# Kernel optimization log

Hardware: AMD Instinct MI355X
Metric: run time of the kernel (lower is better)

## Reference

```python
import jax, jax.numpy as jnp
import numpy as np

B, T, F, H, D, NC = 4096, 16, 64, 512, 15, 2  # batch, seq, feat(+time), hidden, mem window, classes
FX = F - 1  # real feature dim (channel 0 is the time delta)


def setup_inputs() -> dict:
    key = jax.random.key(0)
    ks = jax.random.split(key, 24)
    u = lambda k, shape, s=0.05: jax.random.uniform(k, shape, jnp.float32, -s, s)
    return {
        "inputs": jax.random.normal(ks[0], (B, T, F), jnp.float32),
        "init_proj": u(ks[1], (F, H)),            # self._init, keras random_uniform
        "hc_init": jnp.zeros((1, H), jnp.float32),  # h/c init (zeros initializer)
        # TH_cell: fused LSTM gates [i,f,o,c]
        "Wx": u(ks[2], (FX, 4 * H)),
        "Uh": u(ks[3], (H, 4 * H)),
        "Wt": u(ks[4], (1, 3 * H)),               # time delta -> i,f,o gates
        "b": jnp.zeros((4 * H,), jnp.float32),
        # time-aware gate
        "WxT": u(ks[5], (FX, H)),
        "WtT": u(ks[6], (1, H)),
        "bT": jnp.zeros((H,), jnp.float32),
        # historical attention over str_mem
        "Wa": u(ks[7], (H, H)),
        "Wb": u(ks[8], (H, H)),
        "va": u(ks[9], (H,)),
        "ba": jnp.zeros((H,), jnp.float32),
        # interaction / output combine
        "We": u(ks[10], (H, H)),
        "Wg": u(ks[11], (H, H)),
        "bh": jnp.zeros((H,), jnp.float32),
        # classifier head (Dropout is identity at inference)
        "W1": u(ks[12], (H, 256)),
        "b1": jnp.zeros((256,), jnp.float32),
        "W2": u(ks[13], (256, 32)),
        "b2": jnp.zeros((32,), jnp.float32),
        "W3": u(ks[14], (32, NC)),
        "b3": jnp.zeros((NC,), jnp.float32),
    }


def reference(inputs, init_proj, hc_init, Wx, Uh, Wt, b, WxT, WtT, bT,
              Wa, Wb, va, ba, We, Wg, bh, W1, b1, W2, b2, W3, b3):
    Bn = inputs.shape[0]
    # str_mem init: ones_like(inputs) @ _init, drop last step -> [B, T-1=D, H]
    str_mem = jnp.matmul(jnp.ones_like(inputs), init_proj)[:, :-1]
    h = jnp.broadcast_to(hc_init, (Bn, H))
    c = jnp.broadcast_to(hc_init, (Bn, H))
    x_seq = jnp.transpose(inputs[..., 1:], (1, 0, 2))   # [T, B, FX]
    t_seq = jnp.transpose(inputs[..., :1], (1, 0, 2))   # [T, B, 1]

    def step(carry, xt):
        h, c, mem = carry
        x, t = xt
        z = x @ Wx + h @ Uh + b                      # [B, 4H]
        zi, zf, zo, zc = jnp.split(z, 4, axis=-1)
        ti, tf_, to = jnp.split(t @ Wt, 3, axis=-1)
        i = jax.nn.sigmoid(zi + ti)
        f = jax.nn.sigmoid(zf + tf_)
        o = jax.nn.sigmoid(zo + to)
        chat = jnp.tanh(zc)
        Tg = jax.nn.sigmoid(x @ WxT + jax.nn.sigmoid(t @ WtT) + bT)  # time-aware gate
        c_new = f * c + i * chat + Tg * chat
        h_cur = o * jnp.tanh(c_new)
        # historical attention over sliding memory [B, D, H]
        e = jnp.einsum('bdh,h->bd',
                       jnp.tanh(jnp.einsum('bdh,hk->bdk', mem, Wa)
                                + (h_cur @ Wb + ba)[:, None, :]), va)
        alpha = jax.nn.softmax(e, axis=1)
        ctx = jnp.einsum('bd,bdh->bh', alpha, mem)
        h_new = jnp.tanh(ctx @ We + h_cur @ Wg + bh)
        mem_new = jnp.concatenate([mem[:, 1:], h_new[:, None]], axis=1)
        return (h_new, c_new, mem_new), None

    (h, c, str_mem), _ = jax.lax.scan(step, (h, c, str_mem), (x_seq, t_seq))
    hd = jax.nn.relu(h @ W1 + b1)
    hd = jax.nn.relu(hd @ W2 + b2)
    return jax.nn.softmax(hd @ W3 + b3, axis=-1)
```

## Files before the change

kernel.cpp:

```cpp
#include <hip/hip_runtime.h>
#include <hip/hip_bf16.h>

typedef __bf16 bf16;
typedef __attribute__((ext_vector_type(8))) __bf16 bf16x8;
typedef __attribute__((ext_vector_type(4))) float floatx4;

#define HDIM 512
#define BATCH 4096
#define TSTEPS 16
#define KA 576
#define NR 3584

typedef const __attribute__((address_space(1))) void gvoid;
typedef __attribute__((address_space(3))) void svoid;

__device__ __forceinline__ float ftanh2(float x) {
  return fmaf(-2.f, __builtin_amdgcn_rcpf(exp2f(x * 2.8853900817779268f) + 1.f), 1.f);
}
__device__ __forceinline__ float fsigm2(float x) {
  return __builtin_amdgcn_rcpf(1.f + exp2f(-x * 1.4426950408889634f));
}

__device__ __forceinline__ float waveAllSum(float v) {
#pragma unroll
  for (int off = 32; off > 0; off >>= 1) v += __shfl_xor(v, off, 64);
  return v;
}

__global__ __launch_bounds__(256, 4)
void gemm1_fused(const bf16* __restrict__ A1, const bf16* __restrict__ A2,
                 const bf16* __restrict__ BT,
                 const float* __restrict__ tdT, const float* __restrict__ bvec,
                 const float* __restrict__ WtT, const float* __restrict__ bT,
                 float* __restrict__ cbuf, bf16* __restrict__ hcur,
                 bf16* __restrict__ waSlot, bf16* __restrict__ weSlot) {
  constexpr int BM = 128, BN = 112, BK = 64;
  constexpr int TM = 2, TN = 7;
  __shared__ __align__(16) bf16 As[BM * BK];
  __shared__ __align__(16) bf16 Bs[BN * BK];

  const int tid = threadIdx.x;
  const int lane = tid & 63;
  const int wv = tid >> 6;
  const int quad = lane >> 4;
  const int lr = lane & 15;
  const int bid = blockIdx.x;
  const int xcd = bid & 7;
  const int p = bid >> 3;
  const int n_idx = (xcd << 2) | (p >> 5);
  const int m_idx = p & 31;
  const int m0 = m_idx * BM;
  const int n0 = n_idx * BN;
  const int g8 = lane >> 3;
  const int cl = (lane & 7) ^ g8;

  floatx4 acc[TM][TN];
#pragma unroll
  for (int i = 0; i < TM; ++i)
#pragma unroll
    for (int j = 0; j < TN; ++j) {
      acc[i][j][0] = 0.f; acc[i][j][1] = 0.f; acc[i][j][2] = 0.f; acc[i][j][3] = 0.f;
    }

  {
#pragma unroll
    for (int s = 0; s < 4; ++s) {
      const int g = wv * 4 + s;
      const int r = g * 8 + g8;
      const bf16* src = A1 + (size_t)(m0 + r) * 64 + cl * 8;
      __builtin_amdgcn_global_load_lds((gvoid*)src, (svoid*)&As[g * 512], 16, 0, 0);
    }
#pragma unroll
    for (int s = 0; s < 4; ++s) {
      const int g = wv * 4 + s;
      if (g < 10) {
        const int r = g * 8 + g8;
        const bf16* src = BT + (size_t)(n0 + r) * KA + cl * 8;
        __builtin_amdgcn_global_load_lds((gvoid*)src, (svoid*)&Bs[g * 512], 16, 0, 0);
      }
    }
    __syncthreads();
#pragma unroll
    for (int s = 0; s < 2; ++s) {
      const int lc = s * 4 + quad;
      bf16x8 afr[TM];
      bf16x8 bfr[5];
#pragma unroll
      for (int i = 0; i < TM; ++i) {
        const int r = wv * 32 + i * 16 + lr;
        afr[i] = *reinterpret_cast<const bf16x8*>(&As[r * 64 + ((lc ^ (r & 7)) << 3)]);
      }
#pragma unroll
      for (int j = 0; j < 5; ++j) {
        const int r = j * 16 + lr;
        bfr[j] = *reinterpret_cast<const bf16x8*>(&Bs[r * 64 + ((lc ^ (r & 7)) << 3)]);
      }
#pragma unroll
      for (int i = 0; i < TM; ++i)
#pragma unroll
        for (int j = 0; j < 5; ++j)
          acc[i][j] = __builtin_amdgcn_mfma_f32_16x16x32_bf16(afr[i], bfr[j], acc[i][j], 0, 0, 0);
    }
  }

  constexpr int JMAP[6] = {0, 1, 2, 3, 5, 6};
  for (int kt = 1; kt < KA / BK; ++kt) {
    const int kb = kt * BK;
    __syncthreads();
#pragma unroll
    for (int s = 0; s < 4; ++s) {
      const int g = wv * 4 + s;
      const int r = g * 8 + g8;
      const bf16* src = A2 + (size_t)(m0 + r) * 512 + (kb - 64) + cl * 8;
      __builtin_amdgcn_global_load_lds((gvoid*)src, (svoid*)&As[g * 512], 16, 0, 0);
    }
#pragma unroll
    for (int s = 0; s < 4; ++s) {
      const int g = wv * 4 + s;
      if (g < 14 && g != 8 && g != 9) {
        const int r = g * 8 + g8;
        const bf16* src = BT + (size_t)(n0 + r) * KA + kb + cl * 8;
        __builtin_amdgcn_global_load_lds((gvoid*)src, (svoid*)&Bs[g * 512], 16, 0, 0);
      }
    }
    __syncthreads();
#pragma unroll
    for (int s = 0; s < 2; ++s) {
      const int lc = s * 4 + quad;
      bf16x8 afr[TM];
      bf16x8 bfr[6];
#pragma unroll
      for (int i = 0; i < TM; ++i) {
        const int r = wv * 32 + i * 16 + lr;
        afr[i] = *reinterpret_cast<const bf16x8*>(&As[r * 64 + ((lc ^ (r & 7)) << 3)]);
      }
#pragma unroll
      for (int jj = 0; jj < 6; ++jj) {
        const int r = JMAP[jj] * 16 + lr;
        bfr[jj] = *reinterpret_cast<const bf16x8*>(&Bs[r * 64 + ((lc ^ (r & 7)) << 3)]);
      }
#pragma unroll
      for (int i = 0; i < TM; ++i)
#pragma unroll
        for (int jj = 0; jj < 6; ++jj)
          acc[i][JMAP[jj]] =
              __builtin_amdgcn_mfma_f32_16x16x32_bf16(afr[i], bfr[jj], acc[i][JMAP[jj]], 0, 0, 0);
    }
  }

  const int hcol = n_idx * 16 + lr;
  const float bvi = bvec[hcol], bvf = bvec[512 + hcol];
  const float bvo = bvec[1024 + hcol], bvc = bvec[1536 + hcol];
  const float wtt = WtT[hcol], bt_ = bT[hcol];
#pragma unroll
  for (int i = 0; i < TM; ++i) {
#pragma unroll
    for (int r = 0; r < 4; ++r) {
      const int m = m0 + wv * 32 + i * 16 + quad * 4 + r;
      const float td = tdT[m];
      const size_t o = (size_t)m * 512 + hcol;
      const float c_old = cbuf[o];
      const float i_ = fsigm2(acc[i][0][r] + bvi);
      const float f_ = fsigm2(acc[i][1][r] + bvf);
      const float o_ = fsigm2(acc[i][2][r] + bvo);
      const float ch = ftanh2(acc[i][3][r] + bvc);
      const float tg = fsigm2(acc[i][4][r] + fsigm2(td * wtt) + bt_);
      const float cn = f_ * c_old + (i_ + tg) * ch;
      cbuf[o] = cn;
      hcur[o] = (bf16)(o_ * ftanh2(cn));
      waSlot[o] = (bf16)acc[i][5][r];
      weSlot[o] = (bf16)acc[i][6][r];
    }
  }
}

__global__ __launch_bounds__(256, 4)
void gemm2_kernel(const bf16* __restrict__ hcur, const bf16* __restrict__ wbwgT,
                  const float* __restrict__ baPad, bf16* __restrict__ hWbG) {
  __shared__ __align__(16) bf16 As[128 * 64];
  __shared__ __align__(16) bf16 Bs[64 * 64];

  const int tid = threadIdx.x;
  const int lane = tid & 63;
  const int wv = tid >> 6;
  const int quad = lane >> 4;
  const int lr = lane & 15;
  const int bid = blockIdx.x;
  const int m0 = (bid >> 4) * 128;
  const int n0 = (bid & 15) * 64;
  const int g8 = lane >> 3;
  const int cl = (lane & 7) ^ g8;

  floatx4 acc[2][4];
#pragma unroll
  for (int i = 0; i < 2; ++i)
#pragma unroll
    for (int j = 0; j < 4; ++j) {
      acc[i][j][0] = 0.f; acc[i][j][1] = 0.f; acc[i][j][2] = 0.f; acc[i][j][3] = 0.f;
    }

  for (int kt = 0; kt < 8; ++kt) {
    const int kb = kt * 64;
    __syncthreads();
#pragma unroll
    for (int s = 0; s < 4; ++s) {
      const int g = wv * 4 + s;
      const int r = g * 8 + g8;
      const bf16* src = hcur + (size_t)(m0 + r) * 512 + kb + cl * 8;
      __builtin_amdgcn_global_load_lds((gvoid*)src, (svoid*)&As[g * 512], 16, 0, 0);
    }
#pragma unroll
    for (int s = 0; s < 2; ++s) {
      const int g = wv * 2 + s;
      const int r = g * 8 + g8;
      const bf16* src = wbwgT + (size_t)(n0 + r) * 512 + kb + cl * 8;
      __builtin_amdgcn_global_load_lds((gvoid*)src, (svoid*)&Bs[g * 512], 16, 0, 0);
    }
    __syncthreads();
#pragma unroll
    for (int s = 0; s < 2; ++s) {
      const int lc = s * 4 + quad;
      bf16x8 afr[2];
      bf16x8 bfr[4];
#pragma unroll
      for (int i = 0; i < 2; ++i) {
        const int r = wv * 32 + i * 16 + lr;
        afr[i] = *reinterpret_cast<const bf16x8*>(&As[r * 64 + ((lc ^ (r & 7)) << 3)]);
      }
#pragma unroll
      for (int j = 0; j < 4; ++j) {
        const int r = j * 16 + lr;
        bfr[j] = *reinterpret_cast<const bf16x8*>(&Bs[r * 64 + ((lc ^ (r & 7)) << 3)]);
      }
#pragma unroll
      for (int i = 0; i < 2; ++i)
#pragma unroll
        for (int j = 0; j < 4; ++j)
          acc[i][j] = __builtin_amdgcn_mfma_f32_16x16x32_bf16(afr[i], bfr[j], acc[i][j], 0, 0, 0);
    }
  }

#pragma unroll
  for (int i = 0; i < 2; ++i) {
#pragma unroll
    for (int j = 0; j < 4; ++j) {
      const int n = n0 + j * 16 + lr;
      const float bb = baPad[n];
#pragma unroll
      for (int r = 0; r < 4; ++r) {
        const int m = m0 + wv * 32 + i * 16 + quad * 4 + r;
        hWbG[(size_t)m * 1024 + n] = (bf16)(acc[i][j][r] + bb);
      }
    }
  }
}

template <int BM, int BN>
__global__ __launch_bounds__(256)
void gemm_glds_kernel(const bf16* __restrict__ A1, int ld1, int K1,
                      const bf16* __restrict__ A2, int ld2,
                      const bf16* __restrict__ BT, int K, int mode,
                      float* __restrict__ outF, int ldF, const float* __restrict__ colBias,
                      bf16* __restrict__ outBa, int ldBa, const float* __restrict__ cBias2) {
  constexpr int BK = 32;
  constexpr int WM = BM / 2;
  constexpr int WN = BN / 2;
  constexpr int TM = WM / 16;
  constexpr int TN = WN / 16;
  constexpr int AIW = BM / 64;
  constexpr int BIW = BN / 64;
  __shared__ __align__(16) bf16 As[BM * BK];
  __shared__ __align__(16) bf16 Bs[BN * BK];

  const int tid = threadIdx.x;
  const int lane = tid & 63;
  const int wv = tid >> 6;
  const int wy = wv >> 1;
  const int wx = wv & 1;
  const int quad = lane >> 4;
  const int lr = lane & 15;
  const int m0 = blockIdx.y * BM;
  const int n0 = blockIdx.x * BN;
  const int sw = quad ^ ((lr >> 1) & 3);
  const int srow = lane >> 2;
  const int cl = (lane & 3) ^ ((lane >> 3) & 3);

  floatx4 acc[TM][TN];
#pragma unroll
  for (int i = 0; i < TM; ++i)
#pragma unroll
    for (int j = 0; j < TN; ++j) {
      acc[i][j][0] = 0.f; acc[i][j][1] = 0.f; acc[i][j][2] = 0.f; acc[i][j][3] = 0.f;
    }

  const int kTiles = K / BK;
  for (int kt = 0; kt < kTiles; ++kt) {
    const int kb = kt * BK;
    __syncthreads();
#pragma unroll
    for (int s = 0; s < AIW; ++s) {
      const int rbase = (wv * AIW + s) * 16;
      const int r = rbase + srow;
      const int col = kb + cl * 8;
      const bf16* src = (col < K1) ? (A1 + (size_t)(m0 + r) * ld1 + col)
                                   : (A2 + (size_t)(m0 + r) * ld2 + (col - K1));
      __builtin_amdgcn_global_load_lds((gvoid*)src, (svoid*)&As[rbase * BK], 16, 0, 0);
    }
#pragma unroll
    for (int s = 0; s < BIW; ++s) {
      const int rbase = (wv * BIW + s) * 16;
      const int r = rbase + srow;
      const bf16* src = BT + (size_t)(n0 + r) * K + kb + cl * 8;
      __builtin_amdgcn_global_load_lds((gvoid*)src, (svoid*)&Bs[rbase * BK], 16, 0, 0);
    }
    __syncthreads();
    bf16x8 afr[TM];
    bf16x8 bfr[TN];
#pragma unroll
    for (int i = 0; i < TM; ++i)
      afr[i] = *reinterpret_cast<const bf16x8*>(&As[(wy * WM + i * 16 + lr) * BK + sw * 8]);
#pragma unroll
    for (int j = 0; j < TN; ++j)
      bfr[j] = *reinterpret_cast<const bf16x8*>(&Bs[(wx * WN + j * 16 + lr) * BK + sw * 8]);
#pragma unroll
    for (int i = 0; i < TM; ++i)
#pragma unroll
      for (int j = 0; j < TN; ++j)
        acc[i][j] = __builtin_amdgcn_mfma_f32_16x16x32_bf16(afr[i], bfr[j], acc[i][j], 0, 0, 0);
  }

#pragma unroll
  for (int i = 0; i < TM; ++i) {
#pragma unroll
    for (int j = 0; j < TN; ++j) {
#pragma unroll
      for (int r = 0; r < 4; ++r) {
        int m = m0 + wy * WM + i * 16 + quad * 4 + r;
        int n = n0 + wx * WN + j * 16 + lr;
        float v = acc[i][j][r];
        if (mode == 0) {
          if (colBias != nullptr) v += colBias[n];
          outF[(size_t)m * ldF + n] = v;
        } else {
          v += cBias2[n];
          v = v > 0.f ? v : 0.f;
          outBa[(size_t)m * ldBa + n] = (bf16)v;
        }
      }
    }
  }
}

__global__ void pack_wcombT_kernel(const float* __restrict__ Wx, const float* __restrict__ Uh,
                                   const float* __restrict__ Wt, const float* __restrict__ WxT,
                                   const float* __restrict__ Wa, const float* __restrict__ We,
                                   bf16* __restrict__ out) {
  int idx = blockIdx.x * 256 + threadIdx.x;
  if (idx >= NR * KA) return;
  int n = idx / KA;
  int k = idx - n * KA;
  int blk = n / 112;
  int rem = n - blk * 112;
  int role = rem >> 4;
  int h = blk * 16 + (rem & 15);
  float v = 0.f;
  if (k < 63) {
    if (role < 4) v = Wx[k * 2048 + role * 512 + h];
    else if (role == 4) v = WxT[k * 512 + h];
  } else if (k == 63) {
    if (role < 3) v = Wt[role * 512 + h];
  } else {
    int kh = k - 64;
    if (role < 4) v = Uh[kh * 2048 + role * 512 + h];
    else if (role == 5) v = Wa[kh * 512 + h];
    else if (role == 6) v = We[kh * 512 + h];
  }
  out[idx] = (bf16)v;
}

__global__ void pack_t_kernel(const float* __restrict__ in, bf16* __restrict__ out, int N, int K) {
  int idx = blockIdx.x * 256 + threadIdx.x;
  if (idx >= N * K) return;
  int n = idx / K;
  int j = idx - n * K;
  out[idx] = (bf16)in[(size_t)j * N + n];
}

__global__ __launch_bounds__(512)
void setup_misc_kernel(const float* __restrict__ init_proj, const float* __restrict__ Wa,
                       const float* __restrict__ We, const float* __restrict__ ba,
                       float* __restrict__ sWa, float* __restrict__ sWe,
                       float* __restrict__ baPad) {
  __shared__ float s_sh[HDIM];
  int h = threadIdx.x;
  float acc = 0.f;
  for (int f = 0; f < 64; ++f) acc += init_proj[f * HDIM + h];
  s_sh[h] = acc;
  baPad[h] = ba[h];
  baPad[HDIM + h] = 0.f;
  __syncthreads();
  float a2 = 0.f, a3 = 0.f;
  for (int i = 0; i < HDIM; ++i) {
    a2 += s_sh[i] * Wa[i * HDIM + h];
    a3 += s_sh[i] * We[i * HDIM + h];
  }
  sWa[h] = a2;
  sWe[h] = a3;
}

__global__ void zero_state_kernel(float* __restrict__ c, bf16* __restrict__ h) {
  int idx = blockIdx.x * 256 + threadIdx.x;
  if (idx >= BATCH * HDIM) return;
  c[idx] = 0.f;
  h[idx] = (bf16)0.f;
}

__global__ void build_x_kernel(const float* __restrict__ inputs, bf16* __restrict__ xbuf,
                               float* __restrict__ tdT) {
  int idx = blockIdx.x * 256 + threadIdx.x;
  if (idx >= TSTEPS * BATCH * 64) return;
  int c = idx & 63;
  int bt = idx >> 6;
  int t = bt >> 12;
  int b = bt & 4095;
  float v;
  if (c < 63) {
    v = inputs[(size_t)b * 1024 + t * 64 + 1 + c];
  } else {
    v = inputs[(size_t)b * 1024 + t * 64];
    tdT[t * BATCH + b] = v;
  }
  xbuf[idx] = (bf16)v;
}

template <int K>
__global__ __launch_bounds__(256, 4)
void attention_kernel(const bf16* __restrict__ hWbG,
                      const float* __restrict__ sWa, const float* __restrict__ sWe,
                      const float* __restrict__ va, const float* __restrict__ bh,
                      const bf16* __restrict__ histWa, const bf16* __restrict__ histWe,
                      bf16* __restrict__ hbuf) {
  constexpr float C = 2.8853900817779268f;
  constexpr float L2E = 1.4426950408889634f;
  constexpr int CH = 4;
  constexpr int NC = (K + CH - 1) / CH;
  const int b = blockIdx.x * 4 + (threadIdx.x >> 6);
  const int lane = threadIdx.x & 63;
  const bf16* wbp = hWbG + (size_t)b * 1024 + lane * 8;
  bf16x8 wbv = *reinterpret_cast<const bf16x8*>(wbp);
  bf16x8 wgv = *reinterpret_cast<const bf16x8*>(wbp + 512);

  const bf16* pa = histWa + (size_t)b * HDIM + lane * 8;
  const bf16* pe = histWe + (size_t)b * HDIM + lane * 8;
  constexpr size_t RSTR = (size_t)BATCH * HDIM;

  bf16x8 buf[2][CH];
  if (NC > 0) {
#pragma unroll
    for (int r = 0; r < CH; ++r)
      if (r < K) buf[0][r] = *reinterpret_cast<const bf16x8*>(pa + (size_t)r * RSTR);
    asm volatile("" ::: "memory");
  }

  float wb2[8], vv[8];
  float svv = 0.f;
#pragma unroll
  for (int i = 0; i < 8; ++i) {
    wb2[i] = (float)wbv[i] * C;
    vv[i] = va[lane * 8 + i];
    svv += vv[i];
  }

  float e_init = 0.f;
  if (K < 15) {
    float p = 0.f;
#pragma unroll
    for (int i = 0; i < 8; ++i) {
      float r = __builtin_amdgcn_rcpf(exp2f(fmaf(sWa[lane * 8 + i], C, wb2[i])) + 1.f);
      p = fmaf(vv[i], r, p);
    }
    e_init = waveAllSum(fmaf(-2.f, p, svv));
  }

  float q[K > 0 ? K : 1];
#pragma unroll
  for (int c = 0; c < NC; ++c) {
    if (c + 1 < NC) {
#pragma unroll
      for (int r = 0; r < CH; ++r) {
        const int j = (c + 1) * CH + r;
        if (j < K)
          buf[(c + 1) & 1][r] = *reinterpret_cast<const bf16x8*>(pa + (size_t)j * RSTR);
      }
      asm volatile("" ::: "memory");
    }
#pragma unroll
    for (int r = 0; r < CH; ++r) {
      const int j = c * CH + r;
      if (j < K) {
        float p = 0.f;
#pragma unroll
        for (int i = 0; i < 8; ++i) {
          float t = __builtin_amdgcn_rcpf(
              exp2f(fmaf((float)buf[c & 1][r][i], C, wb2[i])) + 1.f);
          p = fmaf(vv[i], t, p);
        }
        q[j] = fmaf(-2.f, p, svv);
      }
    }
  }

  bf16x8 ebuf[2][CH];
  if (NC > 0) {
#pragma unroll
    for (int r = 0; r < CH; ++r)
      if (r < K) ebuf[0][r] = *reinterpret_cast<const bf16x8*>(pe + (size_t)r * RSTR);
    asm volatile("" ::: "memory");
  }

#pragma unroll
  for (int off = 32; off > 0; off >>= 1) {
#pragma unroll
    for (int j = 0; j < K; ++j) q[j] += __shfl_xor(q[j], off, 64);
  }

  float mx = (K < 15) ? e_init : -1e30f;
#pragma unroll
  for (int j = 0; j < K; ++j) mx = fmaxf(mx, q[j]);
  float winit = (K < 15) ? (float)(15 - K) * exp2f((e_init - mx) * L2E) : 0.f;
  float denom = winit;
  float w[K > 0 ? K : 1];
#pragma unroll
  for (int j = 0; j < K; ++j) {
    w[j] = exp2f((q[j] - mx) * L2E);
    denom += w[j];
  }
  const float inv = __builtin_amdgcn_rcpf(denom);

  float cx[8];
  const float ai = winit * inv;
#pragma unroll
  for (int i = 0; i < 8; ++i) cx[i] = ai * sWe[lane * 8 + i];
#pragma unroll
  for (int c = 0; c < NC; ++c) {
    if (c + 1 < NC) {
#pragma unroll
      for (int r = 0; r < CH; ++r) {
        const int j = (c + 1) * CH + r;
        if (j < K)
          ebuf[(c + 1) & 1][r] = *reinterpret_cast<const bf16x8*>(pe + (size_t)j * RSTR);
      }
      asm volatile("" ::: "memory");
    }
#pragma unroll
    for (int r = 0; r < CH; ++r) {
      const int j = c * CH + r;
      if (j < K) {
        const float aj = w[j] * inv;
#pragma unroll
        for (int i = 0; i < 8; ++i) cx[i] = fmaf(aj, (float)ebuf[c & 1][r][i], cx[i]);
      }
    }
  }

  bf16x8 hnew;
#pragma unroll
  for (int i = 0; i < 8; ++i) {
    float s = cx[i] + (float)wgv[i] + bh[lane * 8 + i];
    float r = __builtin_amdgcn_rcpf(exp2f(s * C) + 1.f);
    hnew[i] = (bf16)fmaf(-2.f, r, 1.f);
  }
  *reinterpret_cast<bf16x8*>(hbuf + (size_t)b * HDIM + lane * 8) = hnew;
}

__global__ __launch_bounds__(256)
void head_kernel(const bf16* __restrict__ hd1, const float* __restrict__ W2,
                 const float* __restrict__ b2, const float* __restrict__ W3,
                 const float* __restrict__ b3, float* __restrict__ out) {
  __shared__ float W2s[256 * 32];
  __shared__ float b2s[32];
  __shared__ float W3s[64];
  __shared__ float b3s[2];
  for (int i = threadIdx.x; i < 256 * 32; i += 256) W2s[i] = W2[i];
  if (threadIdx.x < 32) b2s[threadIdx.x] = b2[threadIdx.x];
  if (threadIdx.x < 64) W3s[threadIdx.x] = W3[threadIdx.x];
  if (threadIdx.x < 2) b3s[threadIdx.x] = b3[threadIdx.x];
  __syncthreads();
  int row = blockIdx.x * 256 + threadIdx.x;
  float acc[32];
#pragma unroll
  for (int j = 0; j < 32; ++j) acc[j] = b2s[j];
  const bf16* hp = hd1 + (size_t)row * 256;
  for (int i = 0; i < 256; ++i) {
    float hv = (float)hp[i];
#pragma unroll
    for (int j = 0; j < 32; ++j) acc[j] += hv * W2s[i * 32 + j];
  }
  float l0 = b3s[0], l1 = b3s[1];
#pragma unroll
  for (int j = 0; j < 32; ++j) {
    float r = fmaxf(acc[j], 0.f);
    l0 += r * W3s[j * 2];
    l1 += r * W3s[j * 2 + 1];
  }
  float m = fmaxf(l0, l1);
  float e0 = __expf(l0 - m), e1 = __expf(l1 - m);
  float inv = 1.f / (e0 + e1);
  out[(size_t)row * 2] = e0 * inv;
  out[(size_t)row * 2 + 1] = e1 * inv;
}

extern "C" void kernel_launch(void* const* d_in, const int* in_sizes, int n_in,
                              void* d_out, int out_size, void* d_ws, size_t ws_size,
                              hipStream_t stream) {
  const float* inputs    = (const float*)d_in[0];
  const float* init_proj = (const float*)d_in[1];
  const float* Wx  = (const float*)d_in[3];
  const float* Uh  = (const float*)d_in[4];
  const float* Wt  = (const float*)d_in[5];
  const float* bv  = (const float*)d_in[6];
  const float* WxT = (const float*)d_in[7];
  const float* WtT = (const float*)d_in[8];
  const float* bT  = (const float*)d_in[9];
  const float* Wa  = (const float*)d_in[10];
  const float* Wb  = (const float*)d_in[11];
  const float* va  = (const float*)d_in[12];
  const float* ba  = (const float*)d_in[13];
  const float* We  = (const float*)d_in[14];
  const float* Wg  = (const float*)d_in[15];
  const float* bh  = (const float*)d_in[16];
  const float* W1  = (const float*)d_in[17];
  const float* b1  = (const float*)d_in[18];
  const float* W2  = (const float*)d_in[19];
  const float* b2  = (const float*)d_in[20];
  const float* W3  = (const float*)d_in[21];
  const float* b3  = (const float*)d_in[22];
  float* out = (float*)d_out;

  char* wp = (char*)d_ws;
  auto carve = [&](size_t bytes) -> void* {
    void* p = (void*)wp;
    wp += (bytes + 255) & ~(size_t)255;
    return p;
  };
  bf16* wcombT = (bf16*)carve((size_t)NR * KA * 2);
  bf16* wbwgT  = (bf16*)carve((size_t)1024 * 512 * 2);
  bf16* w1T    = (bf16*)carve((size_t)256 * 512 * 2);
  float* sWa   = (float*)carve(512 * 4);
  float* sWe   = (float*)carve(512 * 4);
  float* baPad = (float*)carve(1024 * 4);
  bf16* xbuf   = (bf16*)carve((size_t)TSTEPS * BATCH * 64 * 2);
  float* tdT   = (float*)carve((size_t)TSTEPS * BATCH * 4);
  float* cbuf  = (float*)carve((size_t)BATCH * HDIM * 4);
  bf16* hbuf   = (bf16*)carve((size_t)BATCH * HDIM * 2);
  bf16* hcur   = (bf16*)carve((size_t)BATCH * HDIM * 2);
  bf16* hWbG   = (bf16*)carve((size_t)BATCH * 1024 * 2);
  bf16* histWa = (bf16*)carve((size_t)16 * BATCH * HDIM * 2);
  bf16* histWe = (bf16*)carve((size_t)16 * BATCH * HDIM * 2);
  bf16* hd1    = (bf16*)carve((size_t)BATCH * 256 * 2);

  build_x_kernel<<<(TSTEPS * BATCH * 64) / 256, 256, 0, stream>>>(inputs, xbuf, tdT);
  pack_wcombT_kernel<<<(NR * KA + 255) / 256, 256, 0, stream>>>(Wx, Uh, Wt, WxT, Wa, We, wcombT);
  pack_t_kernel<<<(512 * 512) / 256, 256, 0, stream>>>(Wb, wbwgT, 512, 512);
  pack_t_kernel<<<(512 * 512) / 256, 256, 0, stream>>>(Wg, wbwgT + (size_t)512 * 512, 512, 512);
  pack_t_kernel<<<(256 * 512) / 256, 256, 0, stream>>>(W1, w1T, 256, 512);
  setup_misc_kernel<<<1, 512, 0, stream>>>(init_proj, Wa, We, ba, sWa, sWe, baPad);
  zero_state_kernel<<<(BATCH * HDIM) / 256, 256, 0, stream>>>(cbuf, hbuf);

#define ATTN_LAUNCH(KK)                                                              \
  case KK:                                                                           \
    attention_kernel<KK><<<BATCH / 4, 256, 0, stream>>>(hWbG, sWa, sWe, va, bh,      \
                                                        histWa, histWe, hbuf);       \
    break;

  for (int t = 0; t < TSTEPS; ++t) {
    bf16* waSlot = histWa + (size_t)((t + 15) & 15) * BATCH * HDIM;
    bf16* weSlot = histWe + (size_t)((t + 15) & 15) * BATCH * HDIM;
    gemm1_fused<<<1024, 256, 0, stream>>>(
        xbuf + (size_t)t * BATCH * 64, hbuf, wcombT, tdT + (size_t)t * BATCH, bv, WtT, bT,
        cbuf, hcur, waSlot, weSlot);
    gemm2_kernel<<<512, 256, 0, stream>>>(hcur, wbwgT, baPad, hWbG);
    switch (t) {
      ATTN_LAUNCH(0) ATTN_LAUNCH(1) ATTN_LAUNCH(2) ATTN_LAUNCH(3)
      ATTN_LAUNCH(4) ATTN_LAUNCH(5) ATTN_LAUNCH(6) ATTN_LAUNCH(7)
      ATTN_LAUNCH(8) ATTN_LAUNCH(9) ATTN_LAUNCH(10) ATTN_LAUNCH(11)
      ATTN_LAUNCH(12) ATTN_LAUNCH(13) ATTN_LAUNCH(14) ATTN_LAUNCH(15)
    }
  }
#undef ATTN_LAUNCH

  gemm_glds_kernel<64, 128><<<dim3(256 / 128, BATCH / 64), 256, 0, stream>>>(
      hbuf, 512, 512, hbuf, 512, w1T, 512, 3, nullptr, 0, nullptr, hd1, 256, b1);
  head_kernel<<<BATCH / 256, 256, 0, stream>>>(hd1, W2, b2, W3, b3, out);
}
```

Before: 987.0 us.

## Split attention memory slots across two waves per batch row

The attention kernel now assigns two waves to each batch row, with each wave handling alternate memory slots (even or odd j). Partial scores are exchanged through shared memory for the softmax, and the second wave's partial context vector is combined through shared memory before the final tanh. The grid doubles and the launch-bounds occupancy hint rises from 4 to 5. This halves per-wave serial load and exp work and register pressure, aiming to hide memory latency better. The cost is two block-wide barriers, extra LDS traffic, and recomputing the exp weights in both waves.

```diff
diff --git a/kernel.cpp b/kernel.cpp
--- a/kernel.cpp
+++ b/kernel.cpp
@@ -434,7 +434,7 @@
 }
 
 template <int K>
-__global__ __launch_bounds__(256, 4)
+__global__ __launch_bounds__(256, 5)
 void attention_kernel(const bf16* __restrict__ hWbG,
                       const float* __restrict__ sWa, const float* __restrict__ sWe,
                       const float* __restrict__ va, const float* __restrict__ bh,
@@ -443,9 +443,18 @@
   constexpr float C = 2.8853900817779268f;
   constexpr float L2E = 1.4426950408889634f;
   constexpr int CH = 4;
-  constexpr int NC = (K + CH - 1) / CH;
-  const int b = blockIdx.x * 4 + (threadIdx.x >> 6);
-  const int lane = threadIdx.x & 63;
+  constexpr int MAXJ = (K + 1) / 2;
+  constexpr int NC = (MAXJ + CH - 1) / CH;
+  __shared__ float qsh[2][16];
+  __shared__ float cxsh[2][8 * 64];
+
+  const int tid = threadIdx.x;
+  const int lane = tid & 63;
+  const int wv = tid >> 6;
+  const int br = wv >> 1;
+  const int half = wv & 1;
+  const int b = blockIdx.x * 2 + br;
+
   const bf16* wbp = hWbG + (size_t)b * 1024 + lane * 8;
   bf16x8 wbv = *reinterpret_cast<const bf16x8*>(wbp);
   bf16x8 wgv = *reinterpret_cast<const bf16x8*>(wbp + 512);
@@ -454,11 +463,15 @@
   const bf16* pe = histWe + (size_t)b * HDIM + lane * 8;
   constexpr size_t RSTR = (size_t)BATCH * HDIM;
 
-  bf16x8 buf[2][CH];
+  bf16x8 stg[2][CH];
   if (NC > 0) {
 #pragma unroll
-    for (int r = 0; r < CH; ++r)
-      if (r < K) buf[0][r] = *reinterpret_cast<const bf16x8*>(pa + (size_t)r * RSTR);
+    for (int r = 0; r < CH; ++r) {
+      if (r < MAXJ) {
+        const int j = half + 2 * r;
+        if (j < K) stg[0][r] = *reinterpret_cast<const bf16x8*>(pa + (size_t)j * RSTR);
+      }
+    }
     asm volatile("" ::: "memory");
   }
 
@@ -482,95 +495,128 @@
     e_init = waveAllSum(fmaf(-2.f, p, svv));
   }
 
-  float q[K > 0 ? K : 1];
+  float q[MAXJ > 0 ? MAXJ : 1];
 #pragma unroll
   for (int c = 0; c < NC; ++c) {
     if (c + 1 < NC) {
 #pragma unroll
       for (int r = 0; r < CH; ++r) {
-        const int j = (c + 1) * CH + r;
-        if (j < K)
-          buf[(c + 1) & 1][r] = *reinterpret_cast<const bf16x8*>(pa + (size_t)j * RSTR);
+        const int jj = (c + 1) * CH + r;
+        if (jj < MAXJ) {
+          const int j = half + 2 * jj;
+          if (j < K)
+            stg[(c + 1) & 1][r] = *reinterpret_cast<const bf16x8*>(pa + (size_t)j * RSTR);
+        }
       }
       asm volatile("" ::: "memory");
     }
 #pragma unroll
     for (int r = 0; r < CH; ++r) {
-      const int j = c * CH + r;
-      if (j < K) {
-        float p = 0.f;
-#pragma unroll
-        for (int i = 0; i < 8; ++i) {
-          float t = __builtin_amdgcn_rcpf(
-              exp2f(fmaf((float)buf[c & 1][r][i], C, wb2[i])) + 1.f);
-          p = fmaf(vv[i], t, p);
+      const int jj = c * CH + r;
+      if (jj < MAXJ) {
+        const int j = half + 2 * jj;
+        if (j < K) {
+          float p = 0.f;
+#pragma unroll
+          for (int i = 0; i < 8; ++i) {
+            float t = __builtin_amdgcn_rcpf(
+                exp2f(fmaf((float)stg[c & 1][r][i], C, wb2[i])) + 1.f);
+            p = fmaf(vv[i], t, p);
+          }
+          q[jj] = fmaf(-2.f, p, svv);
         }
-        q[j] = fmaf(-2.f, p, svv);
-      }
-    }
-  }
-
-  bf16x8 ebuf[2][CH];
+      }
+    }
+  }
+
   if (NC > 0) {
 #pragma unroll
-    for (int r = 0; r < CH; ++r)
-      if (r < K) ebuf[0][r] = *reinterpret_cast<const bf16x8*>(pe + (size_t)r * RSTR);
+    for (int r = 0; r < CH; ++r) {
+      if (r < MAXJ) {
+        const int j = half + 2 * r;
+        if (j < K) stg[0][r] = *reinterpret_cast<const bf16x8*>(pe + (size_t)j * RSTR);
+      }
+    }
     asm volatile("" ::: "memory");
   }
 
 #pragma unroll
   for (int off = 32; off > 0; off >>= 1) {
 #pragma unroll
-    for (int j = 0; j < K; ++j) q[j] += __shfl_xor(q[j], off, 64);
-  }
+    for (int jj = 0; jj < MAXJ; ++jj)
+      if (half + 2 * jj < K) q[jj] += __shfl_xor(q[jj], off, 64);
+  }
+
+  if (lane == 0) {
+#pragma unroll
+    for (int jj = 0; jj < MAXJ; ++jj) {
+      const int j = half + 2 * jj;
+      if (j < K) qsh[br][j] = q[jj];
+    }
+  }
+  __syncthreads();
 
   float mx = (K < 15) ? e_init : -1e30f;
 #pragma unroll
-  for (int j = 0; j < K; ++j) mx = fmaxf(mx, q[j]);
+  for (int j = 0; j < K; ++j) mx = fmaxf(mx, qsh[br][j]);
   float winit = (K < 15) ? (float)(15 - K) * exp2f((e_init - mx) * L2E) : 0.f;
   float denom = winit;
-  float w[K > 0 ? K : 1];
-#pragma unroll
-  for (int j = 0; j < K; ++j) {
-    w[j] = exp2f((q[j] - mx) * L2E);
-    denom += w[j];
-  }
+#pragma unroll
+  for (int j = 0; j < K; ++j) denom += exp2f((qsh[br][j] - mx) * L2E);
   const float inv = __builtin_amdgcn_rcpf(denom);
 
   float cx[8];
-  const float ai = winit * inv;
-#pragma unroll
-  for (int i = 0; i < 8; ++i) cx[i] = ai * sWe[lane * 8 + i];
+  if (half == 0) {
+    const float ai = winit * inv;
+#pragma unroll
+    for (int i = 0; i < 8; ++i) cx[i] = ai * sWe[lane * 8 + i];
+  } else {
+#pragma unroll
+    for (int i = 0; i < 8; ++i) cx[i] = 0.f;
+  }
 #pragma unroll
   for (int c = 0; c < NC; ++c) {
     if (c + 1 < NC) {
 #pragma unroll
       for (int r = 0; r < CH; ++r) {
-        const int j = (c + 1) * CH + r;
-        if (j < K)
-          ebuf[(c + 1) & 1][r] = *reinterpret_cast<const bf16x8*>(pe + (size_t)j * RSTR);
+        const int jj = (c + 1) * CH + r;
+        if (jj < MAXJ) {
+          const int j = half + 2 * jj;
+          if (j < K)
+            stg[(c + 1) & 1][r] = *reinterpret_cast<const bf16x8*>(pe + (size_t)j * RSTR);
+        }
       }
       asm volatile("" ::: "memory");
     }
 #pragma unroll
     for (int r = 0; r < CH; ++r) {
-      const int j = c * CH + r;
-      if (j < K) {
-        const float aj = w[j] * inv;
-#pragma unroll
-        for (int i = 0; i < 8; ++i) cx[i] = fmaf(aj, (float)ebuf[c & 1][r][i], cx[i]);
-      }
-    }
-  }
-
-  bf16x8 hnew;
-#pragma unroll
-  for (int i = 0; i < 8; ++i) {
-    float s = cx[i] + (float)wgv[i] + bh[lane * 8 + i];
-    float r = __builtin_amdgcn_rcpf(exp2f(s * C) + 1.f);
-    hnew[i] = (bf16)fmaf(-2.f, r, 1.f);
-  }
-  *reinterpret_cast<bf16x8*>(hbuf + (size_t)b * HDIM + lane * 8) = hnew;
+      const int jj = c * CH + r;
+      if (jj < MAXJ) {
+        const int j = half + 2 * jj;
+        if (j < K) {
+          const float aj = exp2f((qsh[br][j] - mx) * L2E) * inv;
+#pragma unroll
+          for (int i = 0; i < 8; ++i) cx[i] = fmaf(aj, (float)stg[c & 1][r][i], cx[i]);
+        }
+      }
+    }
+  }
+
+  if (half == 1) {
+#pragma unroll
+    for (int i = 0; i < 8; ++i) cxsh[br][i * 64 + lane] = cx[i];
+  }
+  __syncthreads();
+  if (half == 0) {
+    bf16x8 hnew;
+#pragma unroll
+    for (int i = 0; i < 8; ++i) {
+      float s = cx[i] + cxsh[br][i * 64 + lane] + (float)wgv[i] + bh[lane * 8 + i];
+      float r = __builtin_amdgcn_rcpf(exp2f(s * C) + 1.f);
+      hnew[i] = (bf16)fmaf(-2.f, r, 1.f);
+    }
+    *reinterpret_cast<bf16x8*>(hbuf + (size_t)b * HDIM + lane * 8) = hnew;
+  }
 }
 
 __global__ __launch_bounds__(256)
@@ -669,7 +715,7 @@
 
 #define ATTN_LAUNCH(KK)                                                              \
   case KK:                                                                           \
-    attention_kernel<KK><<<BATCH / 4, 256, 0, stream>>>(hWbG, sWa, sWe, va, bh,      \
+    attention_kernel<KK><<<BATCH / 2, 256, 0, stream>>>(hWbG, sWa, sWe, va, bh,      \
                                                         histWa, histWe, hbuf);       \
     break;
 
```

Measured after the change: 1.040 ms. 5.4% more time.
